# Kernel tuning notes

Hardware: AMD Instinct MI355X
Metric: run time of the kernel (lower is better)

## Reference

```python
import jax, jax.numpy as jnp
import numpy as np

N = 50000          # nodes
E = 600000         # edges
IN, H, HID = 3, 128, 64   # input_size, embed_size, decoder hidden
L = 5              # block_number (GRU layers)
EPS = 1e-12


def _l2norm(v):
    # F.normalize(v, p=2, dim=1)
    return v / jnp.maximum(jnp.linalg.norm(v, axis=1, keepdims=True), EPS)


def setup_inputs() -> dict:
    key = jax.random.key(0)
    ks = jax.random.split(key, 12)
    s = 0.05
    x = jax.random.normal(ks[0], (N, IN), dtype=jnp.float32)
    edge_idx = jax.random.randint(ks[1], (2, E), 0, N, dtype=jnp.int64)
    return {
        "x": x,
        "edge_idx": edge_idx,
        # encoder embed: Linear(IN, H)
        "W_embed": jax.random.normal(ks[2], (H, IN), dtype=jnp.float32) * s,
        "b_embed": jnp.zeros((H,), dtype=jnp.float32),
        # L stacked GRU(H, H) params, torch gate order (r, z, n)
        "w_ih": jax.random.normal(ks[3], (L, 3 * H, H), dtype=jnp.float32) * s,
        "w_hh": jax.random.normal(ks[4], (L, 3 * H, H), dtype=jnp.float32) * s,
        "b_ih": jax.random.normal(ks[5], (L, 3 * H), dtype=jnp.float32) * s,
        "b_hh": jax.random.normal(ks[6], (L, 3 * H), dtype=jnp.float32) * s,
        # decoder: Linear(H, HID) -> ReLU -> Linear(HID, 1)
        "W_hid": jax.random.normal(ks[7], (HID, H), dtype=jnp.float32) * s,
        "b_hid": jnp.zeros((HID,), dtype=jnp.float32),
        "W_out": jax.random.normal(ks[8], (1, HID), dtype=jnp.float32) * s,
        "b_out": jnp.zeros((1,), dtype=jnp.float32),
    }


def reference(x, edge_idx, W_embed, b_embed, w_ih, w_hh, b_ih, b_hh,
              W_hid, b_hid, W_out, b_out):
    row, col = edge_idx[0], edge_idx[1]
    n = x.shape[0]

    # symmetric degree normalization (deg + 1)^-0.5, identical every layer
    deg = jnp.zeros((n,), dtype=x.dtype).at[col].add(1.0) + 1.0
    dinv = deg ** -0.5
    norm = dinv[row] * dinv[col]            # [E]

    h0 = _l2norm(jax.nn.relu(x @ W_embed.T + b_embed))  # [N, H]

    def step(h, params):
        wih, whh, bih, bhh = params
        # message + add-aggregate: out[col] += norm * h[row]
        msg = norm[:, None] * h[row]                     # [E, H]
        agg = jax.ops.segment_sum(msg, col, num_segments=n)  # [N, H]
        # GRU step: input = agg, hidden = h (torch gate order r, z, n)
        gi = agg @ wih.T + bih                           # [N, 3H]
        gh = h @ whh.T + bhh                             # [N, 3H]
        i_r, i_z, i_n = jnp.split(gi, 3, axis=1)
        h_r, h_z, h_n = jnp.split(gh, 3, axis=1)
        r = jax.nn.sigmoid(i_r + h_r)
        zg = jax.nn.sigmoid(i_z + h_z)
        ng = jnp.tanh(i_n + r * h_n)
        hn = _l2norm((1.0 - zg) * ng + zg * h)
        return hn, hn

    _, hs = jax.lax.scan(step, h0, (w_ih, w_hh, b_ih, b_hh))  # hs: [L, N, H]
    all_h = jnp.concatenate([h0[None], hs], axis=0)           # [L+1, N, H]
    z = jnp.max(all_h, axis=0)                                # layer-wise max-pool

    z = jax.nn.relu(z @ W_hid.T + b_hid)
    return z @ W_out.T + b_out                                # [N, 1]
```

## Files before the change

### kernel.cpp

```cpp
#include <hip/hip_runtime.h>
#include <math.h>


#define NTHREADS 256
#define SCAN_CHUNK 1024

typedef __attribute__((ext_vector_type(8))) short s16x8;
typedef __attribute__((ext_vector_type(4))) float f32x4;

union U8 { s16x8 v; ushort4 h[2]; int4 q; };

__device__ __forceinline__ unsigned short f2bf(float f) {
  union { float f; unsigned u; } x; x.f = f;
  unsigned u = x.u + 0x7FFFu + ((x.u >> 16) & 1u);
  return (unsigned short)(u >> 16);
}
__device__ __forceinline__ float bf2f(unsigned short s) {
  union { unsigned u; float f; } x; x.u = ((unsigned)s) << 16;
  return x.f;
}


__global__ void count_deg(const int* __restrict__ col, int* deg, int E) {
  int e = blockIdx.x * NTHREADS + threadIdx.x;
  if (e < E) atomicAdd(&deg[col[e]], 1);
}

__global__ void block_reduce(const int* __restrict__ cnt, int* __restrict__ bsum,
                             float* __restrict__ dinv, int n) {
  __shared__ int red[NTHREADS];
  int b = blockIdx.x, t = threadIdx.x;
  int base = b * SCAN_CHUNK + t * 4;
  int s = 0;
#pragma unroll
  for (int i = 0; i < 4; ++i) {
    int idx = base + i;
    if (idx < n) {
      int c = cnt[idx];
      s += c;
      dinv[idx] = rsqrtf((float)c + 1.0f);
    }
  }
  red[t] = s;
  __syncthreads();
  for (int off = NTHREADS / 2; off > 0; off >>= 1) {
    if (t < off) red[t] += red[t + off];
    __syncthreads();
  }
  if (t == 0) bsum[b] = red[0];
}

__global__ void scan_partials(const int* __restrict__ bsum, int* __restrict__ boff,
                              int* __restrict__ row_ptr_n, int nb) {
  int t = threadIdx.x;
  int s = (t < nb) ? bsum[t] : 0;
  int orig = s;
#pragma unroll
  for (int off = 1; off < 64; off <<= 1) {
    int v = __shfl_up(s, off);
    if (t >= off) s += v;
  }
  if (t < nb) boff[t] = s - orig;
  if (t == nb - 1) *row_ptr_n = s;
}

__global__ void scan_final(const int* __restrict__ cnt, const int* __restrict__ boff,
                           int* __restrict__ row_ptr, int* __restrict__ cursor, int n) {
  __shared__ int sums[NTHREADS];
  int b = blockIdx.x, t = threadIdx.x;
  int base = b * SCAN_CHUNK + t * 4;
  int v[4];
  int s = 0;
#pragma unroll
  for (int i = 0; i < 4; ++i) { int idx = base + i; v[i] = (idx < n) ? cnt[idx] : 0; s += v[i]; }
  sums[t] = s;
  __syncthreads();
  for (int off = 1; off < NTHREADS; off <<= 1) {
    int a = (t >= off) ? sums[t - off] : 0;
    __syncthreads();
    sums[t] += a;
    __syncthreads();
  }
  int run = boff[b] + sums[t] - s;
#pragma unroll
  for (int i = 0; i < 4; ++i) {
    int idx = base + i;
    if (idx < n) { row_ptr[idx] = run; cursor[idx] = run; }
    run += v[i];
  }
}

__global__ void scatter_edges(const int* __restrict__ row, const int* __restrict__ col,
                              const float* __restrict__ dinv, int* cursor,
                              int* __restrict__ src, float* __restrict__ wgt, int E) {
  int e = blockIdx.x * NTHREADS + threadIdx.x;
  if (e >= E) return;
  int r = row[e], c = col[e];
  int p = atomicAdd(&cursor[c], 1);
  src[p] = r;
  wgt[p] = dinv[r] * dinv[c];
}


__global__ void pack_weights(const float* __restrict__ w_ih, const float* __restrict__ w_hh,
                             unsigned short* __restrict__ out) {
  int idx = blockIdx.x * NTHREADS + threadIdx.x;
  if (idx >= 491520) return;
  int e = idx & 7;
  int lane = (idx >> 3) & 63;
  int ft = (idx >> 9) & 7;
  int v = idx >> 12;
  int g = v % 6;
  int u = v / 6;
  int ks = u & 3;
  int layer = u >> 2;
  int k = 32 * ks + (e & 3) + 4 * ((lane >> 4) & 3) + 16 * (e >> 2);
  int j = 16 * ft + (lane & 15);
  const float* src = (g < 3) ? w_ih : w_hh;
  int gate = g % 3;
  float val = src[(size_t)layer * 49152 + (size_t)(gate * 128 + j) * 128 + k];
  out[idx] = f2bf(val);
}

__global__ void pack_whid(const float* __restrict__ W_hid, unsigned short* __restrict__ out) {
  int idx = blockIdx.x * NTHREADS + threadIdx.x;
  if (idx >= 8192) return;
  int e = idx & 7;
  int lane = (idx >> 3) & 63;
  int ft = (idx >> 9) & 3;
  int ks = idx >> 11;
  int k = 32 * ks + (e & 3) + 4 * ((lane >> 4) & 3) + 16 * (e >> 2);
  int j = 16 * ft + (lane & 15);
  out[idx] = f2bf(W_hid[j * 128 + k]);
}


__global__ void encoder(const float* __restrict__ x, const float* __restrict__ W,
                        const float* __restrict__ b, float* __restrict__ h,
                        unsigned short* __restrict__ hb, unsigned short* __restrict__ zmaxb,
                        int n) {
  int node = blockIdx.x * 4 + (threadIdx.x >> 6);
  int lane = threadIdx.x & 63;
  if (node >= n) return;
  float x0 = x[node * 3 + 0], x1 = x[node * 3 + 1], x2 = x[node * 3 + 2];
  int j0 = lane, j1 = lane + 64;
  float v0 = fmaxf(fmaf(W[j0 * 3 + 2], x2, fmaf(W[j0 * 3 + 1], x1, fmaf(W[j0 * 3], x0, b[j0]))), 0.f);
  float v1 = fmaxf(fmaf(W[j1 * 3 + 2], x2, fmaf(W[j1 * 3 + 1], x1, fmaf(W[j1 * 3], x0, b[j1]))), 0.f);
  float ss = v0 * v0 + v1 * v1;
#pragma unroll
  for (int sh = 32; sh > 0; sh >>= 1) ss += __shfl_down(ss, sh);
  ss = __shfl(ss, 0);
  float sc = 1.0f / fmaxf(sqrtf(ss), 1e-12f);
  size_t base = (size_t)node * 128;
  float o0 = v0 * sc, o1 = v1 * sc;
  h[base + j0] = o0;
  h[base + j1] = o1;
  unsigned short u0 = f2bf(o0), u1 = f2bf(o1);
  hb[base + j0] = u0;
  hb[base + j1] = u1;
  zmaxb[base + j0] = u0;
  zmaxb[base + j1] = u1;
}


__global__ void aggregate(const int* __restrict__ row_ptr, const int* __restrict__ src,
                          const float* __restrict__ wgt, const unsigned short* __restrict__ hb,
                          unsigned short* __restrict__ aggb, int n) {
  int node = blockIdx.x * 4 + (threadIdx.x >> 6);
  int lane = threadIdx.x & 63;
  if (node >= n) return;
  const unsigned* hw = (const unsigned*)hb;
  int pb = row_ptr[node], pe = row_ptr[node + 1];
  float aL[4] = {0.f, 0.f, 0.f, 0.f};
  float aH[4] = {0.f, 0.f, 0.f, 0.f};
  int p = pb;
  for (; p + 8 <= pe; p += 8) {
    unsigned u[8]; float w[8];
#pragma unroll
    for (int i = 0; i < 8; ++i) {
      int s = src[p + i];
      w[i] = wgt[p + i];
      u[i] = hw[(size_t)s * 64 + lane];
    }
#pragma unroll
    for (int i = 0; i < 8; ++i) {
      aL[i & 3] = fmaf(w[i], bf2f((unsigned short)(u[i] & 0xFFFFu)), aL[i & 3]);
      aH[i & 3] = fmaf(w[i], bf2f((unsigned short)(u[i] >> 16)), aH[i & 3]);
    }
  }
  if (p + 4 <= pe) {
    unsigned u[4]; float w[4];
#pragma unroll
    for (int i = 0; i < 4; ++i) {
      int s = src[p + i];
      w[i] = wgt[p + i];
      u[i] = hw[(size_t)s * 64 + lane];
    }
#pragma unroll
    for (int i = 0; i < 4; ++i) {
      aL[i] = fmaf(w[i], bf2f((unsigned short)(u[i] & 0xFFFFu)), aL[i]);
      aH[i] = fmaf(w[i], bf2f((unsigned short)(u[i] >> 16)), aH[i]);
    }
    p += 4;
  }
  for (; p < pe; ++p) {
    int s = src[p];
    float w = wgt[p];
    unsigned u = hw[(size_t)s * 64 + lane];
    aL[0] = fmaf(w, bf2f((unsigned short)(u & 0xFFFFu)), aL[0]);
    aH[0] = fmaf(w, bf2f((unsigned short)(u >> 16)), aH[0]);
  }
  float a0 = (aL[0] + aL[1]) + (aL[2] + aL[3]);
  float a1 = (aH[0] + aH[1]) + (aH[2] + aH[3]);
  unsigned o = ((unsigned)f2bf(a1) << 16) | (unsigned)f2bf(a0);
  ((unsigned*)(aggb + (size_t)node * 128))[lane] = o;
}


__global__ __launch_bounds__(1024) void gru_mfma(
    const unsigned short* __restrict__ aggb, const unsigned short* __restrict__ hbc,
    unsigned short* __restrict__ hbn, float* __restrict__ h,
    unsigned short* __restrict__ zmaxb,
    const int4* __restrict__ wpk, const float* __restrict__ bih,
    const float* __restrict__ bhh, int n, int last) {
  __shared__ unsigned short aggS[64 * 132];
  __shared__ unsigned short hS[64 * 132];
  __shared__ float partS[64 * 8];
  __shared__ float scv[64];
  int tid = threadIdx.x;
  int base = blockIdx.x * 64;
  int w = tid >> 6, l = tid & 63;
  int mh = w & 1, fh = w >> 1;
  int lr = l & 15, lg = l >> 4;
  int jj = fh * 16 + lr;

  float hv[2][4];
#pragma unroll
  for (int mt = 0; mt < 2; ++mt)
#pragma unroll
    for (int e = 0; e < 4; ++e) {
      int gr = base + mh * 32 + mt * 16 + lg * 4 + e;
      if (gr > n - 1) gr = n - 1;
      hv[mt][e] = h[(size_t)gr * 128 + jj];
    }

  ushort4 zv[2];
#pragma unroll
  for (int rep = 0; rep < 2; ++rep) {
    int idx = tid + rep * 1024;
    int row = idx >> 5, c4 = idx & 31;
    int gr = base + row; if (gr > n - 1) gr = n - 1;
    ushort4 ua = *(const ushort4*)(aggb + (size_t)gr * 128 + c4 * 4);
    ushort4 uh = *(const ushort4*)(hbc + (size_t)gr * 128 + c4 * 4);
    zv[rep] = *(const ushort4*)(zmaxb + (size_t)gr * 128 + c4 * 4);
    *(ushort4*)&aggS[row * 132 + c4 * 4] = ua;
    *(ushort4*)&hS[row * 132 + c4 * 4] = uh;
  }
  __syncthreads();

  f32x4 acc[2][6];
#pragma unroll
  for (int mt = 0; mt < 2; ++mt)
#pragma unroll
    for (int g = 0; g < 6; ++g) { acc[mt][g][0] = 0.f; acc[mt][g][1] = 0.f; acc[mt][g][2] = 0.f; acc[mt][g][3] = 0.f; }

#pragma unroll
  for (int ks = 0; ks < 4; ++ks) {
    U8 fa[2], fhh[2];
#pragma unroll
    for (int mt = 0; mt < 2; ++mt) {
      int boff = (mh * 32 + mt * 16 + lr) * 132 + ks * 32 + lg * 4;
      fa[mt].h[0] = *(const ushort4*)&aggS[boff];
      fa[mt].h[1] = *(const ushort4*)&aggS[boff + 16];
      fhh[mt].h[0] = *(const ushort4*)&hS[boff];
      fhh[mt].h[1] = *(const ushort4*)&hS[boff + 16];
    }
#pragma unroll
    for (int g = 0; g < 6; ++g) {
      U8 bw; bw.q = wpk[((ks * 6 + g) * 8 + fh) * 64 + l];
      const U8& a0 = (g < 3) ? fa[0] : fhh[0];
      const U8& a1 = (g < 3) ? fa[1] : fhh[1];
      acc[0][g] = __builtin_amdgcn_mfma_f32_16x16x32_bf16(a0.v, bw.v, acc[0][g], 0, 0, 0);
      acc[1][g] = __builtin_amdgcn_mfma_f32_16x16x32_bf16(a1.v, bw.v, acc[1][g], 0, 0, 0);
    }
  }

  float br = bih[jj], bz = bih[128 + jj], bn = bih[256 + jj];
  float cr = bhh[jj], cz = bhh[128 + jj], cn = bhh[256 + jj];
  float hn_out[2][4];
#pragma unroll
  for (int mt = 0; mt < 2; ++mt)
#pragma unroll
    for (int e = 0; e < 4; ++e) {
      int row = mh * 32 + mt * 16 + lg * 4 + e;
      float ir = acc[mt][0][e], iz = acc[mt][1][e], inn = acc[mt][2][e];
      float hr = acc[mt][3][e], hz = acc[mt][4][e], hnv = acc[mt][5][e];
      float r = 1.f / (1.f + __expf(-(ir + hr + br + cr)));
      float z = 1.f / (1.f + __expf(-(iz + hz + bz + cz)));
      float ng = tanhf(inn + bn + r * (hnv + cn));
      float hn = (1.f - z) * ng + z * hv[mt][e];
      hn_out[mt][e] = hn;
      float p = hn * hn;
      p += __shfl_xor(p, 1);
      p += __shfl_xor(p, 2);
      p += __shfl_xor(p, 4);
      p += __shfl_xor(p, 8);
      if (lr == 0) partS[row * 8 + fh] = p;
    }
  __syncthreads();
  if (tid < 64) {
    float ss = 0.f;
#pragma unroll
    for (int f = 0; f < 8; ++f) ss += partS[tid * 8 + f];
    scv[tid] = 1.f / fmaxf(sqrtf(ss), 1e-12f);
  }
  __syncthreads();

#pragma unroll
  for (int mt = 0; mt < 2; ++mt)
#pragma unroll
    for (int e = 0; e < 4; ++e) {
      int row = mh * 32 + mt * 16 + lg * 4 + e;
      float v = hn_out[mt][e] * scv[row];
      int gr = base + row;
      if (!last && gr < n) h[(size_t)gr * 128 + jj] = v;
      aggS[row * 132 + jj] = f2bf(v);
    }
  __syncthreads();

#pragma unroll
  for (int rep = 0; rep < 2; ++rep) {
    int idx = tid + rep * 1024;
    int row = idx >> 5, c4 = idx & 31;
    int gr = base + row;
    if (gr < n) {
      ushort4 hv4 = *(const ushort4*)&aggS[row * 132 + c4 * 4];
      ushort4 z4 = zv[rep];
      z4.x = (bf2f(hv4.x) > bf2f(z4.x)) ? hv4.x : z4.x;
      z4.y = (bf2f(hv4.y) > bf2f(z4.y)) ? hv4.y : z4.y;
      z4.z = (bf2f(hv4.z) > bf2f(z4.z)) ? hv4.z : z4.z;
      z4.w = (bf2f(hv4.w) > bf2f(z4.w)) ? hv4.w : z4.w;
      *(ushort4*)(zmaxb + (size_t)gr * 128 + c4 * 4) = z4;
      if (!last) *(ushort4*)(hbn + (size_t)gr * 128 + c4 * 4) = hv4;
    }
  }
}


__global__ __launch_bounds__(256) void decoder_mfma(
    const unsigned short* __restrict__ zb, const int4* __restrict__ wdpk,
    const float* __restrict__ bh, const float* __restrict__ Wo,
    const float* __restrict__ bo, float* __restrict__ out, int n) {
  __shared__ unsigned short zS[64 * 132];
  int tid = threadIdx.x;
  int base = blockIdx.x * 64;
#pragma unroll
  for (int rep = 0; rep < 8; ++rep) {
    int idx = tid + rep * 256;
    int row = idx >> 5, c4 = idx & 31;
    int gr = base + row; if (gr > n - 1) gr = n - 1;
    ushort4 uz = *(const ushort4*)(zb + (size_t)gr * 128 + c4 * 4);
    *(ushort4*)&zS[row * 132 + c4 * 4] = uz;
  }
  __syncthreads();
  int w = tid >> 6, l = tid & 63;
  int lr = l & 15, lg = l >> 4;
  f32x4 acc[4];
#pragma unroll
  for (int ft = 0; ft < 4; ++ft) { acc[ft][0] = 0.f; acc[ft][1] = 0.f; acc[ft][2] = 0.f; acc[ft][3] = 0.f; }
#pragma unroll
  for (int ks = 0; ks < 4; ++ks) {
    U8 fz;
    int boff = (w * 16 + lr) * 132 + ks * 32 + lg * 4;
    fz.h[0] = *(const ushort4*)&zS[boff];
    fz.h[1] = *(const ushort4*)&zS[boff + 16];
#pragma unroll
    for (int ft = 0; ft < 4; ++ft) {
      U8 bw; bw.q = wdpk[(ks * 4 + ft) * 64 + l];
      acc[ft] = __builtin_amdgcn_mfma_f32_16x16x32_bf16(fz.v, bw.v, acc[ft], 0, 0, 0);
    }
  }
  float s[4] = {0.f, 0.f, 0.f, 0.f};
#pragma unroll
  for (int ft = 0; ft < 4; ++ft) {
    int j = ft * 16 + lr;
    float bj = bh[j], wj = Wo[j];
#pragma unroll
    for (int e = 0; e < 4; ++e) {
      float hid = fmaxf(acc[ft][e] + bj, 0.f);
      s[e] = fmaf(hid, wj, s[e]);
    }
  }
#pragma unroll
  for (int e = 0; e < 4; ++e) {
    float v = s[e];
    v += __shfl_xor(v, 1);
    v += __shfl_xor(v, 2);
    v += __shfl_xor(v, 4);
    v += __shfl_xor(v, 8);
    if (lr == 0) {
      int gr = base + w * 16 + lg * 4 + e;
      if (gr < n) out[gr] = v + bo[0];
    }
  }
}


extern "C" void kernel_launch(void* const* d_in, const int* in_sizes, int n_in,
                              void* d_out, int out_size, void* d_ws, size_t ws_size,
                              hipStream_t stream) {
  const float* x       = (const float*)d_in[0];
  const int*   edge    = (const int*)d_in[1];
  const float* W_embed = (const float*)d_in[2];
  const float* b_embed = (const float*)d_in[3];
  const float* w_ih    = (const float*)d_in[4];
  const float* w_hh    = (const float*)d_in[5];
  const float* b_ih    = (const float*)d_in[6];
  const float* b_hh    = (const float*)d_in[7];
  const float* W_hid   = (const float*)d_in[8];
  const float* b_hid   = (const float*)d_in[9];
  const float* W_out   = (const float*)d_in[10];
  const float* b_out   = (const float*)d_in[11];
  float* out = (float*)d_out;

  const int N = in_sizes[0] / 3;
  const int E = in_sizes[1] / 2;
  const int NB = (N + SCAN_CHUNK - 1) / SCAN_CHUNK;

  char* ws = (char*)d_ws;
  size_t off = 0;
  auto alloc = [&](size_t bytes) -> void* {
    void* p = ws + off;
    off = (off + bytes + 511) & ~(size_t)511;
    return p;
  };
  int*   deg     = (int*)alloc((size_t)N * 4);
  float* dinv    = (float*)alloc((size_t)N * 4);
  int*   row_ptr = (int*)alloc((size_t)(N + 1) * 4);
  int*   cursor  = (int*)alloc((size_t)N * 4);
  int*   bsum    = (int*)alloc((size_t)NB * 4);
  int*   boff    = (int*)alloc((size_t)NB * 4);
  int*   srcv    = (int*)alloc((size_t)E * 4);
  float* wgtv    = (float*)alloc((size_t)E * 4);
  unsigned short* wpack  = (unsigned short*)alloc((size_t)491520 * 2);
  unsigned short* wdpack = (unsigned short*)alloc((size_t)8192 * 2);
  float* h       = (float*)alloc((size_t)N * 128 * 4);
  unsigned short* hb0   = (unsigned short*)alloc((size_t)N * 128 * 2);
  unsigned short* hb1   = (unsigned short*)alloc((size_t)N * 128 * 2);
  unsigned short* aggb  = (unsigned short*)alloc((size_t)N * 128 * 2);
  unsigned short* zmaxb = (unsigned short*)alloc((size_t)N * 128 * 2);

  const int* erow = edge;
  const int* ecol = edge + E;

  hipMemsetAsync(deg, 0, (size_t)N * 4, stream);
  count_deg<<<(E + NTHREADS - 1) / NTHREADS, NTHREADS, 0, stream>>>(ecol, deg, E);
  block_reduce<<<NB, NTHREADS, 0, stream>>>(deg, bsum, dinv, N);
  scan_partials<<<1, 64, 0, stream>>>(bsum, boff, row_ptr + N, NB);
  scan_final<<<NB, NTHREADS, 0, stream>>>(deg, boff, row_ptr, cursor, N);
  scatter_edges<<<(E + NTHREADS - 1) / NTHREADS, NTHREADS, 0, stream>>>(erow, ecol, dinv, cursor, srcv, wgtv, E);

  pack_weights<<<(491520 + NTHREADS - 1) / NTHREADS, NTHREADS, 0, stream>>>(w_ih, w_hh, wpack);
  pack_whid<<<32, NTHREADS, 0, stream>>>(W_hid, wdpack);

  encoder<<<(N + 3) / 4, NTHREADS, 0, stream>>>(x, W_embed, b_embed, h, hb0, zmaxb, N);

  unsigned short* hbb[2] = {hb0, hb1};
  for (int l = 0; l < 5; ++l) {
    aggregate<<<(N + 3) / 4, NTHREADS, 0, stream>>>(row_ptr, srcv, wgtv, hbb[l & 1], aggb, N);
    gru_mfma<<<(N + 63) / 64, 1024, 0, stream>>>(
        aggb, hbb[l & 1], hbb[(l + 1) & 1], h, zmaxb,
        (const int4*)(wpack + (size_t)l * 98304),
        b_ih + (size_t)l * 384, b_hh + (size_t)l * 384, N, (l == 4) ? 1 : 0);
  }

  decoder_mfma<<<(N + 63) / 64, NTHREADS, 0, stream>>>(
      zmaxb, (const int4*)wdpack, b_hid, W_out, b_out, out, N);
}
```

Measured before the change: 477.8 us.

## Drop fp32 hidden state and defer layer max-pool to decoder

Removes the fp32 copy of the hidden state. The GRU now reads the previous hidden value from the bf16 tile already in shared memory, which cuts fp32 loads and stores in every layer. The running max-pool buffer, updated each layer, is replaced by keeping all six bf16 layer outputs and taking the max once inside the decoder. In exchange the GRU blend runs on bf16-rounded hidden values, adding precision loss, and memory use grows to six N×128 buffers, while the decoder now reads six tensors.

```diff
diff --git a/kernel.cpp b/kernel.cpp
--- a/kernel.cpp
+++ b/kernel.cpp
@@ -136,9 +136,7 @@
 
 
 __global__ void encoder(const float* __restrict__ x, const float* __restrict__ W,
-                        const float* __restrict__ b, float* __restrict__ h,
-                        unsigned short* __restrict__ hb, unsigned short* __restrict__ zmaxb,
-                        int n) {
+                        const float* __restrict__ b, unsigned short* __restrict__ hb, int n) {
   int node = blockIdx.x * 4 + (threadIdx.x >> 6);
   int lane = threadIdx.x & 63;
   if (node >= n) return;
@@ -152,14 +150,8 @@
   ss = __shfl(ss, 0);
   float sc = 1.0f / fmaxf(sqrtf(ss), 1e-12f);
   size_t base = (size_t)node * 128;
-  float o0 = v0 * sc, o1 = v1 * sc;
-  h[base + j0] = o0;
-  h[base + j1] = o1;
-  unsigned short u0 = f2bf(o0), u1 = f2bf(o1);
-  hb[base + j0] = u0;
-  hb[base + j1] = u1;
-  zmaxb[base + j0] = u0;
-  zmaxb[base + j1] = u1;
+  hb[base + j0] = f2bf(v0 * sc);
+  hb[base + j1] = f2bf(v1 * sc);
 }
 
 
@@ -219,10 +211,9 @@
 
 __global__ __launch_bounds__(1024) void gru_mfma(
     const unsigned short* __restrict__ aggb, const unsigned short* __restrict__ hbc,
-    unsigned short* __restrict__ hbn, float* __restrict__ h,
-    unsigned short* __restrict__ zmaxb,
+    unsigned short* __restrict__ hbn,
     const int4* __restrict__ wpk, const float* __restrict__ bih,
-    const float* __restrict__ bhh, int n, int last) {
+    const float* __restrict__ bhh, int n) {
   __shared__ unsigned short aggS[64 * 132];
   __shared__ unsigned short hS[64 * 132];
   __shared__ float partS[64 * 8];
@@ -234,17 +225,6 @@
   int lr = l & 15, lg = l >> 4;
   int jj = fh * 16 + lr;
 
-  float hv[2][4];
-#pragma unroll
-  for (int mt = 0; mt < 2; ++mt)
-#pragma unroll
-    for (int e = 0; e < 4; ++e) {
-      int gr = base + mh * 32 + mt * 16 + lg * 4 + e;
-      if (gr > n - 1) gr = n - 1;
-      hv[mt][e] = h[(size_t)gr * 128 + jj];
-    }
-
-  ushort4 zv[2];
 #pragma unroll
   for (int rep = 0; rep < 2; ++rep) {
     int idx = tid + rep * 1024;
@@ -252,7 +232,6 @@
     int gr = base + row; if (gr > n - 1) gr = n - 1;
     ushort4 ua = *(const ushort4*)(aggb + (size_t)gr * 128 + c4 * 4);
     ushort4 uh = *(const ushort4*)(hbc + (size_t)gr * 128 + c4 * 4);
-    zv[rep] = *(const ushort4*)(zmaxb + (size_t)gr * 128 + c4 * 4);
     *(ushort4*)&aggS[row * 132 + c4 * 4] = ua;
     *(ushort4*)&hS[row * 132 + c4 * 4] = uh;
   }
@@ -298,7 +277,8 @@
       float r = 1.f / (1.f + __expf(-(ir + hr + br + cr)));
       float z = 1.f / (1.f + __expf(-(iz + hz + bz + cz)));
       float ng = tanhf(inn + bn + r * (hnv + cn));
-      float hn = (1.f - z) * ng + z * hv[mt][e];
+      float hv = bf2f(hS[row * 132 + jj]);
+      float hn = (1.f - z) * ng + z * hv;
       hn_out[mt][e] = hn;
       float p = hn * hn;
       p += __shfl_xor(p, 1);
@@ -321,10 +301,7 @@
 #pragma unroll
     for (int e = 0; e < 4; ++e) {
       int row = mh * 32 + mt * 16 + lg * 4 + e;
-      float v = hn_out[mt][e] * scv[row];
-      int gr = base + row;
-      if (!last && gr < n) h[(size_t)gr * 128 + jj] = v;
-      aggS[row * 132 + jj] = f2bf(v);
+      aggS[row * 132 + jj] = f2bf(hn_out[mt][e] * scv[row]);
     }
   __syncthreads();
 
@@ -335,32 +312,41 @@
     int gr = base + row;
     if (gr < n) {
       ushort4 hv4 = *(const ushort4*)&aggS[row * 132 + c4 * 4];
-      ushort4 z4 = zv[rep];
-      z4.x = (bf2f(hv4.x) > bf2f(z4.x)) ? hv4.x : z4.x;
-      z4.y = (bf2f(hv4.y) > bf2f(z4.y)) ? hv4.y : z4.y;
-      z4.z = (bf2f(hv4.z) > bf2f(z4.z)) ? hv4.z : z4.z;
-      z4.w = (bf2f(hv4.w) > bf2f(z4.w)) ? hv4.w : z4.w;
-      *(ushort4*)(zmaxb + (size_t)gr * 128 + c4 * 4) = z4;
-      if (!last) *(ushort4*)(hbn + (size_t)gr * 128 + c4 * 4) = hv4;
+      *(ushort4*)(hbn + (size_t)gr * 128 + c4 * 4) = hv4;
     }
   }
 }
 
 
 __global__ __launch_bounds__(256) void decoder_mfma(
-    const unsigned short* __restrict__ zb, const int4* __restrict__ wdpk,
-    const float* __restrict__ bh, const float* __restrict__ Wo,
-    const float* __restrict__ bo, float* __restrict__ out, int n) {
+    const unsigned short* __restrict__ h0, const unsigned short* __restrict__ h1,
+    const unsigned short* __restrict__ h2, const unsigned short* __restrict__ h3,
+    const unsigned short* __restrict__ h4, const unsigned short* __restrict__ h5,
+    const int4* __restrict__ wdpk, const float* __restrict__ bh,
+    const float* __restrict__ Wo, const float* __restrict__ bo,
+    float* __restrict__ out, int n) {
   __shared__ unsigned short zS[64 * 132];
   int tid = threadIdx.x;
   int base = blockIdx.x * 64;
+  const unsigned short* hp[6] = {h0, h1, h2, h3, h4, h5};
 #pragma unroll
   for (int rep = 0; rep < 8; ++rep) {
     int idx = tid + rep * 256;
     int row = idx >> 5, c4 = idx & 31;
     int gr = base + row; if (gr > n - 1) gr = n - 1;
-    ushort4 uz = *(const ushort4*)(zb + (size_t)gr * 128 + c4 * 4);
-    *(ushort4*)&zS[row * 132 + c4 * 4] = uz;
+    size_t o = (size_t)gr * 128 + c4 * 4;
+    ushort4 uu[6];
+#pragma unroll
+    for (int li = 0; li < 6; ++li) uu[li] = *(const ushort4*)(hp[li] + o);
+    ushort4 m = uu[0];
+#pragma unroll
+    for (int li = 1; li < 6; ++li) {
+      m.x = (bf2f(uu[li].x) > bf2f(m.x)) ? uu[li].x : m.x;
+      m.y = (bf2f(uu[li].y) > bf2f(m.y)) ? uu[li].y : m.y;
+      m.z = (bf2f(uu[li].z) > bf2f(m.z)) ? uu[li].z : m.z;
+      m.w = (bf2f(uu[li].w) > bf2f(m.w)) ? uu[li].w : m.w;
+    }
+    *(ushort4*)&zS[row * 132 + c4 * 4] = m;
   }
   __syncthreads();
   int w = tid >> 6, l = tid & 63;
@@ -444,11 +430,9 @@
   float* wgtv    = (float*)alloc((size_t)E * 4);
   unsigned short* wpack  = (unsigned short*)alloc((size_t)491520 * 2);
   unsigned short* wdpack = (unsigned short*)alloc((size_t)8192 * 2);
-  float* h       = (float*)alloc((size_t)N * 128 * 4);
-  unsigned short* hb0   = (unsigned short*)alloc((size_t)N * 128 * 2);
-  unsigned short* hb1   = (unsigned short*)alloc((size_t)N * 128 * 2);
-  unsigned short* aggb  = (unsigned short*)alloc((size_t)N * 128 * 2);
-  unsigned short* zmaxb = (unsigned short*)alloc((size_t)N * 128 * 2);
+  unsigned short* aggb   = (unsigned short*)alloc((size_t)N * 128 * 2);
+  unsigned short* hbs[6];
+  for (int i = 0; i < 6; ++i) hbs[i] = (unsigned short*)alloc((size_t)N * 128 * 2);
 
   const int* erow = edge;
   const int* ecol = edge + E;
@@ -463,17 +447,17 @@
   pack_weights<<<(491520 + NTHREADS - 1) / NTHREADS, NTHREADS, 0, stream>>>(w_ih, w_hh, wpack);
   pack_whid<<<32, NTHREADS, 0, stream>>>(W_hid, wdpack);
 
-  encoder<<<(N + 3) / 4, NTHREADS, 0, stream>>>(x, W_embed, b_embed, h, hb0, zmaxb, N);
-
-  unsigned short* hbb[2] = {hb0, hb1};
+  encoder<<<(N + 3) / 4, NTHREADS, 0, stream>>>(x, W_embed, b_embed, hbs[0], N);
+
   for (int l = 0; l < 5; ++l) {
-    aggregate<<<(N + 3) / 4, NTHREADS, 0, stream>>>(row_ptr, srcv, wgtv, hbb[l & 1], aggb, N);
+    aggregate<<<(N + 3) / 4, NTHREADS, 0, stream>>>(row_ptr, srcv, wgtv, hbs[l], aggb, N);
     gru_mfma<<<(N + 63) / 64, 1024, 0, stream>>>(
-        aggb, hbb[l & 1], hbb[(l + 1) & 1], h, zmaxb,
+        aggb, hbs[l], hbs[l + 1],
         (const int4*)(wpack + (size_t)l * 98304),
-        b_ih + (size_t)l * 384, b_hh + (size_t)l * 384, N, (l == 4) ? 1 : 0);
+        b_ih + (size_t)l * 384, b_hh + (size_t)l * 384, N);
   }
 
   decoder_mfma<<<(N + 63) / 64, NTHREADS, 0, stream>>>(
-      zmaxb, (const int4*)wdpack, b_hid, W_out, b_out, out, N);
-}
+      hbs[0], hbs[1], hbs[2], hbs[3], hbs[4], hbs[5],
+      (const int4*)wdpack, b_hid, W_out, b_out, out, N);
+}
```

Measured after the change: 426.1 us. 10.8% less time.
